# Performance work log

Hardware: AMD Instinct MI355X
Metric: run time of the kernel (lower is better)

## Reference

```python
import jax, jax.numpy as jnp
import numpy as np

N_DIM = 512
HIDDEN = 512


def setup_inputs() -> dict:
    key = jax.random.key(0)
    ks = jax.random.split(key, 9)
    s = 0.02
    x = jax.random.normal(ks[0], (4, 4096, N_DIM), dtype=jnp.float32)
    Wq = jax.random.normal(ks[1], (N_DIM, HIDDEN), dtype=jnp.float32) * s
    bq = jnp.zeros((HIDDEN,), dtype=jnp.float32)
    Wk = jax.random.normal(ks[2], (N_DIM, HIDDEN), dtype=jnp.float32) * s
    bk = jnp.zeros((HIDDEN,), dtype=jnp.float32)
    Wv = jax.random.normal(ks[3], (N_DIM, HIDDEN), dtype=jnp.float32) * s
    bv = jnp.zeros((HIDDEN,), dtype=jnp.float32)
    Wo = jax.random.normal(ks[4], (HIDDEN, N_DIM), dtype=jnp.float32) * s
    bo = jnp.zeros((N_DIM,), dtype=jnp.float32)
    return {"x": x, "Wq": Wq, "bq": bq, "Wk": Wk, "bk": bk,
            "Wv": Wv, "bv": bv, "Wo": Wo, "bo": bo}


def reference(x, Wq, bq, Wk, bk, Wv, bv, Wo, bo):
    # x: [B, S, n_dim]
    q = jnp.einsum('bsd,dh->bsh', x, Wq) + bq  # [B,S,H]
    k = jnp.einsum('bsd,dh->bsh', x, Wk) + bk
    v = jnp.einsum('bsd,dh->bsh', x, Wv) + bv
    # NOTE: original module uses UNSCALED scores (no 1/sqrt(d))
    scores = jnp.einsum('bqh,bkh->bqk', q, k)  # [B,S,S]
    attn = jax.nn.softmax(scores, axis=-1)
    y = jnp.einsum('bqk,bkh->bqh', attn, v)
    return jnp.einsum('bsh,hd->bsd', y, Wo) + bo
```

## Files before the change

kernel.cpp:

```cpp
#include <hip/hip_runtime.h>
#include <hip/hip_bf16.h>

typedef _Float16 h8 __attribute__((ext_vector_type(8)));
typedef __bf16   b8 __attribute__((ext_vector_type(8)));
typedef float    f4 __attribute__((ext_vector_type(4)));

#define B_    4
#define S_    4096
#define D_    512
#define ROWS_ (B_ * S_)
#define NQKV_ 1536
#define BR    64
#define BC2   64
#define NIT2  (S_ / BC2)
#define KP3   520
#define KT3   (BC2 * KP3)
#define PP3   72
#define YP    520
#define MSH   (30.0f * 1.4426950408889634f)
#define L2E   1.4426950408889634f

__device__ __forceinline__ void gl_lds16(const void* src, void* dst) {
    __builtin_amdgcn_global_load_lds(
        (const __attribute__((address_space(1))) unsigned int*)src,
        (__attribute__((address_space(3))) unsigned int*)dst, 16, 0, 0);
}

__global__ __launch_bounds__(256) void convert_all(
    const float* __restrict__ x,
    const float* __restrict__ Wq, const float* __restrict__ Wk, const float* __restrict__ Wv,
    const float* __restrict__ bq, const float* __restrict__ bk, const float* __restrict__ bv,
    const float* __restrict__ Wo,
    _Float16* __restrict__ xh, _Float16* __restrict__ wqkvT, _Float16* __restrict__ woT,
    float* __restrict__ bqkv)
{
    long i0 = (long)blockIdx.x * blockDim.x + threadIdx.x;
    long stride = (long)gridDim.x * blockDim.x;
    const long NX  = (long)ROWS_ * D_;
    const long NW  = (long)D_ * NQKV_;
    const long NWO = (long)D_ * D_;

    for (long i = i0; i < NX; i += stride) xh[i] = (_Float16)x[i];

    for (long i = i0; i < NW; i += stride) {
        long n = i >> 9, k = i & 511;
        long which = n >> 9, nn = n & 511;
        const float* W = (which == 0) ? Wq : (which == 1) ? Wk : Wv;
        wqkvT[i] = (_Float16)W[k * 512 + nn];
    }
    for (long i = i0; i < NWO; i += stride) {
        long n = i >> 9, k = i & 511;
        woT[i] = (_Float16)Wo[k * 512 + n];
    }
    for (long i = i0; i < NQKV_; i += stride) {
        long which = i >> 9, nn = i & 511;
        const float* bb = (which == 0) ? bq : (which == 1) ? bk : bv;
        bqkv[i] = bb[nn];
    }
}

template <bool OUT_F16>
__global__ __launch_bounds__(512) void gemm_bt(
    const _Float16* __restrict__ A, const _Float16* __restrict__ BT,
    const float* __restrict__ bias, void* __restrict__ Cout,
    int M, int N, int K, __bf16* __restrict__ vPout)
{
    __shared__ _Float16 As[2][128 * 32];
    __shared__ _Float16 Bs[2][256 * 32];

    int tid = threadIdx.x;
    int w = tid >> 6, lane = tid & 63, quad = lane >> 4, l16 = lane & 15;
    long row0 = (long)blockIdx.x * 128, col0 = (long)blockIdx.y * 256;
    int wr = (w >> 2) * 64, wc = (w & 3) * 64;

    f4 acc[4][4];
    for (int i = 0; i < 4; i++)
        for (int j = 0; j < 4; j++) acc[i][j] = (f4){0.f, 0.f, 0.f, 0.f};

    const int lrow = lane >> 2;
    const int lcol = (lane & 3) * 8;
    const int NT = K >> 5;

    gl_lds16(A  + (row0 + w * 16 + lrow) * K + lcol,        As[0] + w * 512);
    gl_lds16(BT + (col0 + w * 16 + lrow) * K + lcol,        Bs[0] + w * 512);
    gl_lds16(BT + (col0 + (w + 8) * 16 + lrow) * K + lcol,  Bs[0] + (w + 8) * 512);
    __syncthreads();

    for (int t = 0; t < NT; ++t) {
        const int cur = t & 1;
        if (t + 1 < NT) {
            const int k1 = (t + 1) * 32;
            gl_lds16(A  + (row0 + w * 16 + lrow) * K + k1 + lcol,        As[cur ^ 1] + w * 512);
            gl_lds16(BT + (col0 + w * 16 + lrow) * K + k1 + lcol,        Bs[cur ^ 1] + w * 512);
            gl_lds16(BT + (col0 + (w + 8) * 16 + lrow) * K + k1 + lcol,  Bs[cur ^ 1] + (w + 8) * 512);
        }
        h8 af[4], bf[4];
        for (int i = 0; i < 4; i++) af[i] = *(const h8*)(As[cur] + (wr + i * 16 + l16) * 32 + quad * 8);
        for (int j = 0; j < 4; j++) bf[j] = *(const h8*)(Bs[cur] + (wc + j * 16 + l16) * 32 + quad * 8);
        for (int i = 0; i < 4; i++)
            for (int j = 0; j < 4; j++)
                acc[i][j] = __builtin_amdgcn_mfma_f32_16x16x32_f16(af[i], bf[j], acc[i][j], 0, 0, 0);
        __builtin_amdgcn_sched_barrier(0);
        asm volatile("s_waitcnt vmcnt(0)");
        asm volatile("s_waitcnt lgkmcnt(0)");
        __builtin_amdgcn_s_barrier();
        __builtin_amdgcn_sched_barrier(0);
    }

    if (OUT_F16 && vPout != nullptr && col0 >= 1024) {
        for (int i = 0; i < 4; i++) {
            long row = row0 + wr + i * 16 + quad * 4;
            int bb   = (int)(row >> 12);
            int s    = (int)(row & 4095);
            int kt32 = s >> 5;
            int qq   = (s >> 3) & 3;
            int k3   = s & 7;
            for (int j = 0; j < 4; j++) {
                int dglob = (int)(col0 - 1024) + wc + j * 16;
                int dt = dglob >> 4;
                long off = (((long)bb * 128 + kt32) * 32 + dt) * 512
                         + (qq * 16 + l16) * 8 + k3;
                union { __bf16 h[4]; uint2 u2; } pk;
                for (int r = 0; r < 4; r++)
                    pk.h[r] = (__bf16)(acc[i][j][r] + bias[col0 + wc + j * 16 + l16]);
                *(uint2*)(vPout + off) = pk.u2;
            }
        }
    } else {
        for (int i = 0; i < 4; i++)
            for (int j = 0; j < 4; j++)
                for (int r = 0; r < 4; r++) {
                    long row = row0 + wr + i * 16 + quad * 4 + r;
                    long col = col0 + wc + j * 16 + l16;
                    float v = acc[i][j][r] + bias[col];
                    if (OUT_F16) ((_Float16*)Cout)[row * N + col] = (_Float16)v;
                    else         ((float*)Cout)[row * N + col]    = v;
                }
    }
}

__global__ __launch_bounds__(512, 2) void attn_kernel(const _Float16* __restrict__ qkv,
                                                      const __bf16* __restrict__ vP,
                                                      const _Float16* __restrict__ woT,
                                                      const float* __restrict__ bo,
                                                      float* __restrict__ out)
{
    __shared__ _Float16 Ks[2 * KT3];
    __shared__ __bf16   Ps[2 * BR * PP3];
    __shared__ float    lpart[2][BR];

    const int tid = threadIdx.x;
    const int w = tid >> 6, lane = tid & 63, quad = lane >> 4, l16 = lane & 15;

    const int bid = blockIdx.x;
    const int xcd = bid & 7;
    const int b = xcd >> 1;
    const long q0 = (long)((xcd & 1) * 32 + (bid >> 3)) * BR;
    const long rowBase = (long)b * S_;

    const _Float16* kbase = qkv + rowBase * NQKV_ + 512;

#pragma unroll
    for (int i = 0; i < 8; i++) {
        int r = w * 8 + i;
        gl_lds16(kbase + (long)r * NQKV_ + lane * 8, Ks + r * KP3);
    }

    if (w < 4) {
        const int rs0 = (w & 1) * 32;
        const int kg0 = (w >> 1) * 32;

        h8 Qf0[16], Qf1[16];
        {
            const _Float16* q0p = qkv + (rowBase + q0 + rs0 + l16) * NQKV_;
            const _Float16* q1p = q0p + 16 * NQKV_;
#pragma unroll
            for (int ks = 0; ks < 16; ks++) {
                Qf0[ks] = *(const h8*)(q0p + ks * 32 + quad * 8);
                Qf1[ks] = *(const h8*)(q1p + ks * 32 + quad * 8);
            }
        }
        float lo0[4] = {0.f, 0.f, 0.f, 0.f};
        float lo1[4] = {0.f, 0.f, 0.f, 0.f};

        __syncthreads();

        for (int kt = 0; kt < NIT2; kt++) {
            if (kt + 1 < NIT2) {
                const _Float16* kn = kbase + (long)(kt + 1) * BC2 * NQKV_;
                _Float16* kd = Ks + ((kt + 1) & 1) * KT3;
#pragma unroll
                for (int i = 0; i < 8; i++) {
                    int r = w * 8 + i;
                    gl_lds16(kn + (long)r * NQKV_ + lane * 8, kd + r * KP3);
                }
            }
            f4 S[2][2][2];
#pragma unroll
            for (int a = 0; a < 2; a++)
#pragma unroll
                for (int c = 0; c < 2; c++)
#pragma unroll
                    for (int d = 0; d < 2; d++) S[a][c][d] = (f4){0.f, 0.f, 0.f, 0.f};
            const _Float16* kr0 = Ks + (kt & 1) * KT3 + (kg0 + l16) * KP3 + quad * 8;
            const _Float16* kr1 = kr0 + 16 * KP3;
            __builtin_amdgcn_s_setprio(1);
#pragma unroll
            for (int ks = 0; ks < 8; ks++) {
                h8 a0 = *(const h8*)(kr0 + ks * 32);
                h8 a1 = *(const h8*)(kr0 + (ks + 8) * 32);
                h8 c0 = *(const h8*)(kr1 + ks * 32);
                h8 c1 = *(const h8*)(kr1 + (ks + 8) * 32);
                S[0][0][0] = __builtin_amdgcn_mfma_f32_16x16x32_f16(Qf0[ks],     a0, S[0][0][0], 0, 0, 0);
                S[1][0][0] = __builtin_amdgcn_mfma_f32_16x16x32_f16(Qf1[ks],     a0, S[1][0][0], 0, 0, 0);
                S[0][1][0] = __builtin_amdgcn_mfma_f32_16x16x32_f16(Qf0[ks],     c0, S[0][1][0], 0, 0, 0);
                S[1][1][0] = __builtin_amdgcn_mfma_f32_16x16x32_f16(Qf1[ks],     c0, S[1][1][0], 0, 0, 0);
                S[0][0][1] = __builtin_amdgcn_mfma_f32_16x16x32_f16(Qf0[ks + 8], a1, S[0][0][1], 0, 0, 0);
                S[1][0][1] = __builtin_amdgcn_mfma_f32_16x16x32_f16(Qf1[ks + 8], a1, S[1][0][1], 0, 0, 0);
                S[0][1][1] = __builtin_amdgcn_mfma_f32_16x16x32_f16(Qf0[ks + 8], c1, S[0][1][1], 0, 0, 0);
                S[1][1][1] = __builtin_amdgcn_mfma_f32_16x16x32_f16(Qf1[ks + 8], c1, S[1][1][1], 0, 0, 0);
            }
            __builtin_amdgcn_s_setprio(0);
            __bf16* ps = Ps + (kt & 1) * (BR * PP3);
#pragma unroll
            for (int r = 0; r < 4; r++) {
                float p00 = exp2f((S[0][0][0][r] + S[0][0][1][r]) * L2E - MSH);
                float p01 = exp2f((S[0][1][0][r] + S[0][1][1][r]) * L2E - MSH);
                float p10 = exp2f((S[1][0][0][r] + S[1][0][1][r]) * L2E - MSH);
                float p11 = exp2f((S[1][1][0][r] + S[1][1][1][r]) * L2E - MSH);
                __bf16 b00 = (__bf16)p00, b01 = (__bf16)p01;
                __bf16 b10 = (__bf16)p10, b11 = (__bf16)p11;
                int r0 = (rs0 + quad * 4 + r) * PP3;
                int r1 = (rs0 + 16 + quad * 4 + r) * PP3;
                ps[r0 + kg0 + l16]      = b00;
                ps[r0 + kg0 + 16 + l16] = b01;
                ps[r1 + kg0 + l16]      = b10;
                ps[r1 + kg0 + 16 + l16] = b11;
                lo0[r] += (float)b00 + (float)b01;
                lo1[r] += (float)b10 + (float)b11;
            }
            __builtin_amdgcn_sched_barrier(0);
            asm volatile("s_waitcnt vmcnt(0)");
            asm volatile("s_waitcnt lgkmcnt(0)");
            __builtin_amdgcn_s_barrier();
            __builtin_amdgcn_sched_barrier(0);
        }

#pragma unroll
        for (int r = 0; r < 4; r++)
#pragma unroll
            for (int m = 1; m < 16; m <<= 1) {
                lo0[r] += __shfl_xor(lo0[r], m, 16);
                lo1[r] += __shfl_xor(lo1[r], m, 16);
            }
        if (l16 == 0)
            for (int r = 0; r < 4; r++) {
                lpart[w >> 1][rs0 + quad * 4 + r]      = lo0[r];
                lpart[w >> 1][rs0 + 16 + quad * 4 + r] = lo1[r];
            }
        __syncthreads();
        __syncthreads();
    } else {
        const int cv = w - 4;
        const __bf16* vpbase = vP + ((long)b * 128 * 32 + cv * 8) * 512 + lane * 8;

        f4 O[4][8];
#pragma unroll
        for (int rt = 0; rt < 4; rt++)
#pragma unroll
            for (int ct = 0; ct < 8; ct++) O[rt][ct] = (f4){0.f, 0.f, 0.f, 0.f};
        b8 vreg[16];

        __syncthreads();

        for (int kt = 0; kt < NIT2; kt++) {
            if (kt + 1 < NIT2) {
                const _Float16* kn = kbase + (long)(kt + 1) * BC2 * NQKV_;
                _Float16* kd = Ks + ((kt + 1) & 1) * KT3;
#pragma unroll
                for (int i = 0; i < 8; i++) {
                    int r = w * 8 + i;
                    gl_lds16(kn + (long)r * NQKV_ + lane * 8, kd + r * KP3);
                }
            }
            __builtin_amdgcn_sched_barrier(0);
            if (kt > 0) {
                if (kt < NIT2 - 1) asm volatile("s_waitcnt vmcnt(8)");
                else               asm volatile("s_waitcnt vmcnt(0)");
                const __bf16* ps = Ps + ((kt - 1) & 1) * (BR * PP3);
                __builtin_amdgcn_s_setprio(1);
#pragma unroll
                for (int rt = 0; rt < 4; rt++) {
                    b8 pa0 = *(const b8*)(ps + (rt * 16 + l16) * PP3 + quad * 8);
                    b8 pa1 = *(const b8*)(ps + (rt * 16 + l16) * PP3 + 32 + quad * 8);
#pragma unroll
                    for (int ct = 0; ct < 8; ct++) {
                        O[rt][ct] = __builtin_amdgcn_mfma_f32_16x16x32_bf16(pa0, vreg[ct],     O[rt][ct], 0, 0, 0);
                        O[rt][ct] = __builtin_amdgcn_mfma_f32_16x16x32_bf16(pa1, vreg[8 + ct], O[rt][ct], 0, 0, 0);
                    }
                }
                __builtin_amdgcn_s_setprio(0);
            }
            {
                const __bf16* vs0 = vpbase + (long)(2 * kt) * (32 * 512);
#pragma unroll
                for (int ct = 0; ct < 8; ct++) {
                    vreg[ct]     = *(const b8*)(vs0 + ct * 512);
                    vreg[8 + ct] = *(const b8*)(vs0 + 32 * 512 + ct * 512);
                }
            }
            __builtin_amdgcn_sched_barrier(0);
            asm volatile("s_waitcnt vmcnt(16)");
            asm volatile("s_waitcnt lgkmcnt(0)");
            __builtin_amdgcn_s_barrier();
            __builtin_amdgcn_sched_barrier(0);
        }
        asm volatile("s_waitcnt vmcnt(0)");
        {
            const __bf16* ps = Ps + ((NIT2 - 1) & 1) * (BR * PP3);
#pragma unroll
            for (int rt = 0; rt < 4; rt++) {
                b8 pa0 = *(const b8*)(ps + (rt * 16 + l16) * PP3 + quad * 8);
                b8 pa1 = *(const b8*)(ps + (rt * 16 + l16) * PP3 + 32 + quad * 8);
#pragma unroll
                for (int ct = 0; ct < 8; ct++) {
                    O[rt][ct] = __builtin_amdgcn_mfma_f32_16x16x32_bf16(pa0, vreg[ct],     O[rt][ct], 0, 0, 0);
                    O[rt][ct] = __builtin_amdgcn_mfma_f32_16x16x32_bf16(pa1, vreg[8 + ct], O[rt][ct], 0, 0, 0);
                }
            }
        }
        __syncthreads();

        {
            _Float16* y_lds = Ks;
#pragma unroll
            for (int rt = 0; rt < 4; rt++) {
                f4 l0 = *(const f4*)(&lpart[0][rt * 16 + quad * 4]);
                f4 l1 = *(const f4*)(&lpart[1][rt * 16 + quad * 4]);
                float li[4];
                for (int r = 0; r < 4; r++) li[r] = 1.f / (l0[r] + l1[r]);
                for (int ct = 0; ct < 8; ct++)
                    for (int r = 0; r < 4; r++)
                        y_lds[(rt * 16 + quad * 4 + r) * YP + cv * 128 + ct * 16 + l16] =
                            (_Float16)(O[rt][ct][r] * li[r]);
            }
        }
        __syncthreads();
    }

    {
        const _Float16* y_lds = Ks;
        f4 acc[4][4];
#pragma unroll
        for (int i = 0; i < 4; i++)
#pragma unroll
            for (int j = 0; j < 4; j++) acc[i][j] = (f4){0.f, 0.f, 0.f, 0.f};
        const _Float16* wb = woT + (long)(w * 64 + l16) * 512 + quad * 8;
#pragma unroll
        for (int ks = 0; ks < 16; ks++) {
            h8 af[4], bf[4];
#pragma unroll
            for (int i = 0; i < 4; i++)
                af[i] = *(const h8*)(y_lds + (i * 16 + l16) * YP + ks * 32 + quad * 8);
#pragma unroll
            for (int j = 0; j < 4; j++)
                bf[j] = *(const h8*)(wb + (long)j * 16 * 512 + ks * 32);
#pragma unroll
            for (int i = 0; i < 4; i++)
#pragma unroll
                for (int j = 0; j < 4; j++)
                    acc[i][j] = __builtin_amdgcn_mfma_f32_16x16x32_f16(af[i], bf[j], acc[i][j], 0, 0, 0);
        }
#pragma unroll
        for (int i = 0; i < 4; i++)
#pragma unroll
            for (int j = 0; j < 4; j++)
                for (int r = 0; r < 4; r++) {
                    long row = rowBase + q0 + i * 16 + quad * 4 + r;
                    int col = w * 64 + j * 16 + l16;
                    out[row * 512 + col] = acc[i][j][r] + bo[col];
                }
    }
}

extern "C" void kernel_launch(void* const* d_in, const int* in_sizes, int n_in,
                              void* d_out, int out_size, void* d_ws, size_t ws_size,
                              hipStream_t stream)
{
    const float* x  = (const float*)d_in[0];
    const float* Wq = (const float*)d_in[1];
    const float* bq = (const float*)d_in[2];
    const float* Wk = (const float*)d_in[3];
    const float* bk = (const float*)d_in[4];
    const float* Wv = (const float*)d_in[5];
    const float* bv = (const float*)d_in[6];
    const float* Wo = (const float*)d_in[7];
    const float* bo = (const float*)d_in[8];
    float* out = (float*)d_out;

    char* ws = (char*)d_ws;
    _Float16* xh    = (_Float16*)(ws);
    _Float16* qkv   = (_Float16*)(ws + 16777216);
    __bf16*   vP    = (__bf16*)(ws + 67108864);
    _Float16* wqkvT = (_Float16*)(ws + 100663296);
    _Float16* woT   = (_Float16*)(ws + 102236160);
    float*    bqkv  = (float*)(ws + 102760448);

    convert_all<<<2048, 256, 0, stream>>>(x, Wq, Wk, Wv, bq, bk, bv, Wo,
                                          xh, wqkvT, woT, bqkv);

    dim3 g1(128, 6);
    gemm_bt<true><<<g1, 512, 0, stream>>>(xh, wqkvT, bqkv, qkv, ROWS_, NQKV_, D_, vP);

    attn_kernel<<<256, 512, 0, stream>>>(qkv, vP, woT, bo, out);
}
```

Measured before the change: 295.7 us.

## Fuse convert, QKV GEMM and attention into one cooperative persistent kernel

Merges the three separate launches (conversion, QKV projection GEMM, attention plus output projection) into a single cooperative kernel of 256 blocks, separated by grid-wide syncs. This removes launch gaps and kernel-boundary drains between stages. In exchange, the GEMM stage now runs 768 tiles over 256 persistent blocks with a large static LDS allocation, and the conversion stage uses fewer threads. Grid syncs add their own overhead.

```diff
diff --git a/kernel.cpp b/kernel.cpp
--- a/kernel.cpp
+++ b/kernel.cpp
@@ -1,5 +1,8 @@
 #include <hip/hip_runtime.h>
 #include <hip/hip_bf16.h>
+#include <hip/hip_cooperative_groups.h>
+
+namespace cg = cooperative_groups;
 
 typedef _Float16 h8 __attribute__((ext_vector_type(8)));
 typedef __bf16   b8 __attribute__((ext_vector_type(8)));
@@ -26,269 +29,307 @@
         (__attribute__((address_space(3))) unsigned int*)dst, 16, 0, 0);
 }
 
-__global__ __launch_bounds__(256) void convert_all(
+__global__ __launch_bounds__(512, 2) void fused_all(
     const float* __restrict__ x,
-    const float* __restrict__ Wq, const float* __restrict__ Wk, const float* __restrict__ Wv,
-    const float* __restrict__ bq, const float* __restrict__ bk, const float* __restrict__ bv,
-    const float* __restrict__ Wo,
-    _Float16* __restrict__ xh, _Float16* __restrict__ wqkvT, _Float16* __restrict__ woT,
-    float* __restrict__ bqkv)
+    const float* __restrict__ Wq, const float* __restrict__ bq,
+    const float* __restrict__ Wk, const float* __restrict__ bk,
+    const float* __restrict__ Wv, const float* __restrict__ bv,
+    const float* __restrict__ Wo, const float* __restrict__ bo,
+    _Float16* __restrict__ xh, _Float16* __restrict__ wqkvT,
+    _Float16* __restrict__ woT, float* __restrict__ bqkv,
+    _Float16* __restrict__ qkv, __bf16* __restrict__ vP,
+    float* __restrict__ out)
 {
-    long i0 = (long)blockIdx.x * blockDim.x + threadIdx.x;
-    long stride = (long)gridDim.x * blockDim.x;
-    const long NX  = (long)ROWS_ * D_;
-    const long NW  = (long)D_ * NQKV_;
-    const long NWO = (long)D_ * D_;
-
-    for (long i = i0; i < NX; i += stride) xh[i] = (_Float16)x[i];
-
-    for (long i = i0; i < NW; i += stride) {
-        long n = i >> 9, k = i & 511;
-        long which = n >> 9, nn = n & 511;
-        const float* W = (which == 0) ? Wq : (which == 1) ? Wk : Wv;
-        wqkvT[i] = (_Float16)W[k * 512 + nn];
+    __shared__ __align__(16) char smem[152064];
+
+    cg::grid_group gg = cg::this_grid();
+    const int tid = threadIdx.x;
+    const int bid = blockIdx.x;
+    const int w = tid >> 6, lane = tid & 63, quad = lane >> 4, l16 = lane & 15;
+
+    {
+        long i0 = (long)bid * 512 + tid;
+        const long stride = 256 * 512;
+        const long NX  = (long)ROWS_ * D_;
+        const long NW  = (long)D_ * NQKV_;
+        const long NWO = (long)D_ * D_;
+
+        for (long i = i0; i < NX; i += stride) xh[i] = (_Float16)x[i];
+
+        for (long i = i0; i < NW; i += stride) {
+            long n = i >> 9, k = i & 511;
+            long which = n >> 9, nn = n & 511;
+            const float* W = (which == 0) ? Wq : (which == 1) ? Wk : Wv;
+            wqkvT[i] = (_Float16)W[k * 512 + nn];
+        }
+        for (long i = i0; i < NWO; i += stride) {
+            long n = i >> 9, k = i & 511;
+            woT[i] = (_Float16)Wo[k * 512 + n];
+        }
+        for (long i = i0; i < NQKV_; i += stride) {
+            long which = i >> 9, nn = i & 511;
+            const float* bb = (which == 0) ? bq : (which == 1) ? bk : bv;
+            bqkv[i] = bb[nn];
+        }
     }
-    for (long i = i0; i < NWO; i += stride) {
-        long n = i >> 9, k = i & 511;
-        woT[i] = (_Float16)Wo[k * 512 + n];
+    __threadfence();
+    gg.sync();
+
+    {
+        _Float16* As = (_Float16*)smem;
+        _Float16* Bs = (_Float16*)(smem + 16384);
+        const int lrow = lane >> 2;
+        const int lcol = (lane & 3) * 8;
+        const int wr = (w >> 2) * 64, wc = (w & 3) * 64;
+
+        for (int tile = bid; tile < 768; tile += 256) {
+            const long row0 = (long)(tile & 127) * 128;
+            const long col0 = (long)(tile >> 7) * 256;
+
+            f4 acc[4][4];
+#pragma unroll
+            for (int i = 0; i < 4; i++)
+#pragma unroll
+                for (int j = 0; j < 4; j++) acc[i][j] = (f4){0.f, 0.f, 0.f, 0.f};
+
+            gl_lds16(xh    + (row0 + w * 16 + lrow) * 512 + lcol,       As + w * 512);
+            gl_lds16(wqkvT + (col0 + w * 16 + lrow) * 512 + lcol,       Bs + w * 512);
+            gl_lds16(wqkvT + (col0 + (w + 8) * 16 + lrow) * 512 + lcol, Bs + (w + 8) * 512);
+            __syncthreads();
+
+            for (int t = 0; t < 16; ++t) {
+                const int cur = t & 1;
+                if (t + 1 < 16) {
+                    const int k1 = (t + 1) * 32;
+                    gl_lds16(xh    + (row0 + w * 16 + lrow) * 512 + k1 + lcol,       As + (cur ^ 1) * 4096 + w * 512);
+                    gl_lds16(wqkvT + (col0 + w * 16 + lrow) * 512 + k1 + lcol,       Bs + (cur ^ 1) * 8192 + w * 512);
+                    gl_lds16(wqkvT + (col0 + (w + 8) * 16 + lrow) * 512 + k1 + lcol, Bs + (cur ^ 1) * 8192 + (w + 8) * 512);
+                }
+                h8 af[4], bf[4];
+#pragma unroll
+                for (int i = 0; i < 4; i++) af[i] = *(const h8*)(As + cur * 4096 + (wr + i * 16 + l16) * 32 + quad * 8);
+#pragma unroll
+                for (int j = 0; j < 4; j++) bf[j] = *(const h8*)(Bs + cur * 8192 + (wc + j * 16 + l16) * 32 + quad * 8);
+#pragma unroll
+                for (int i = 0; i < 4; i++)
+#pragma unroll
+                    for (int j = 0; j < 4; j++)
+                        acc[i][j] = __builtin_amdgcn_mfma_f32_16x16x32_f16(af[i], bf[j], acc[i][j], 0, 0, 0);
+                __builtin_amdgcn_sched_barrier(0);
+                asm volatile("s_waitcnt vmcnt(0)");
+                asm volatile("s_waitcnt lgkmcnt(0)");
+                __builtin_amdgcn_s_barrier();
+                __builtin_amdgcn_sched_barrier(0);
+            }
+
+            if (col0 >= 1024) {
+#pragma unroll
+                for (int i = 0; i < 4; i++) {
+                    long row = row0 + wr + i * 16 + quad * 4;
+                    int bb   = (int)(row >> 12);
+                    int s    = (int)(row & 4095);
+                    int kt32 = s >> 5;
+                    int qq   = (s >> 3) & 3;
+                    int k3   = s & 7;
+#pragma unroll
+                    for (int j = 0; j < 4; j++) {
+                        int dglob = (int)(col0 - 1024) + wc + j * 16;
+                        int dt = dglob >> 4;
+                        long off = (((long)bb * 128 + kt32) * 32 + dt) * 512
+                                 + (qq * 16 + l16) * 8 + k3;
+                        union { __bf16 h[4]; uint2 u2; } pk;
+                        for (int r = 0; r < 4; r++)
+                            pk.h[r] = (__bf16)(acc[i][j][r] + bqkv[col0 + wc + j * 16 + l16]);
+                        *(uint2*)(vP + off) = pk.u2;
+                    }
+                }
+            } else {
+#pragma unroll
+                for (int i = 0; i < 4; i++)
+#pragma unroll
+                    for (int j = 0; j < 4; j++)
+                        for (int r = 0; r < 4; r++) {
+                            long row = row0 + wr + i * 16 + quad * 4 + r;
+                            long col = col0 + wc + j * 16 + l16;
+                            qkv[row * NQKV_ + col] = (_Float16)(acc[i][j][r] + bqkv[col]);
+                        }
+            }
+            __syncthreads();
+        }
     }
-    for (long i = i0; i < NQKV_; i += stride) {
-        long which = i >> 9, nn = i & 511;
-        const float* bb = (which == 0) ? bq : (which == 1) ? bk : bv;
-        bqkv[i] = bb[nn];
-    }
-}
-
-template <bool OUT_F16>
-__global__ __launch_bounds__(512) void gemm_bt(
-    const _Float16* __restrict__ A, const _Float16* __restrict__ BT,
-    const float* __restrict__ bias, void* __restrict__ Cout,
-    int M, int N, int K, __bf16* __restrict__ vPout)
-{
-    __shared__ _Float16 As[2][128 * 32];
-    __shared__ _Float16 Bs[2][256 * 32];
-
-    int tid = threadIdx.x;
-    int w = tid >> 6, lane = tid & 63, quad = lane >> 4, l16 = lane & 15;
-    long row0 = (long)blockIdx.x * 128, col0 = (long)blockIdx.y * 256;
-    int wr = (w >> 2) * 64, wc = (w & 3) * 64;
-
-    f4 acc[4][4];
-    for (int i = 0; i < 4; i++)
-        for (int j = 0; j < 4; j++) acc[i][j] = (f4){0.f, 0.f, 0.f, 0.f};
-
-    const int lrow = lane >> 2;
-    const int lcol = (lane & 3) * 8;
-    const int NT = K >> 5;
-
-    gl_lds16(A  + (row0 + w * 16 + lrow) * K + lcol,        As[0] + w * 512);
-    gl_lds16(BT + (col0 + w * 16 + lrow) * K + lcol,        Bs[0] + w * 512);
-    gl_lds16(BT + (col0 + (w + 8) * 16 + lrow) * K + lcol,  Bs[0] + (w + 8) * 512);
-    __syncthreads();
-
-    for (int t = 0; t < NT; ++t) {
-        const int cur = t & 1;
-        if (t + 1 < NT) {
-            const int k1 = (t + 1) * 32;
-            gl_lds16(A  + (row0 + w * 16 + lrow) * K + k1 + lcol,        As[cur ^ 1] + w * 512);
-            gl_lds16(BT + (col0 + w * 16 + lrow) * K + k1 + lcol,        Bs[cur ^ 1] + w * 512);
-            gl_lds16(BT + (col0 + (w + 8) * 16 + lrow) * K + k1 + lcol,  Bs[cur ^ 1] + (w + 8) * 512);
-        }
-        h8 af[4], bf[4];
-        for (int i = 0; i < 4; i++) af[i] = *(const h8*)(As[cur] + (wr + i * 16 + l16) * 32 + quad * 8);
-        for (int j = 0; j < 4; j++) bf[j] = *(const h8*)(Bs[cur] + (wc + j * 16 + l16) * 32 + quad * 8);
-        for (int i = 0; i < 4; i++)
-            for (int j = 0; j < 4; j++)
-                acc[i][j] = __builtin_amdgcn_mfma_f32_16x16x32_f16(af[i], bf[j], acc[i][j], 0, 0, 0);
-        __builtin_amdgcn_sched_barrier(0);
-        asm volatile("s_waitcnt vmcnt(0)");
-        asm volatile("s_waitcnt lgkmcnt(0)");
-        __builtin_amdgcn_s_barrier();
-        __builtin_amdgcn_sched_barrier(0);
-    }
-
-    if (OUT_F16 && vPout != nullptr && col0 >= 1024) {
-        for (int i = 0; i < 4; i++) {
-            long row = row0 + wr + i * 16 + quad * 4;
-            int bb   = (int)(row >> 12);
-            int s    = (int)(row & 4095);
-            int kt32 = s >> 5;
-            int qq   = (s >> 3) & 3;
-            int k3   = s & 7;
-            for (int j = 0; j < 4; j++) {
-                int dglob = (int)(col0 - 1024) + wc + j * 16;
-                int dt = dglob >> 4;
-                long off = (((long)bb * 128 + kt32) * 32 + dt) * 512
-                         + (qq * 16 + l16) * 8 + k3;
-                union { __bf16 h[4]; uint2 u2; } pk;
-                for (int r = 0; r < 4; r++)
-                    pk.h[r] = (__bf16)(acc[i][j][r] + bias[col0 + wc + j * 16 + l16]);
-                *(uint2*)(vPout + off) = pk.u2;
-            }
-        }
-    } else {
-        for (int i = 0; i < 4; i++)
-            for (int j = 0; j < 4; j++)
+    __threadfence();
+    gg.sync();
+
+    {
+        _Float16* Ks = (_Float16*)smem;
+        __bf16*   Ps = (__bf16*)(smem + 133120);
+        float*    lp = (float*)(smem + 151552);
+
+        const int xcd = bid & 7;
+        const int b = xcd >> 1;
+        const long q0 = (long)((xcd & 1) * 32 + (bid >> 3)) * BR;
+        const long rowBase = (long)b * S_;
+
+        const _Float16* kbase = qkv + rowBase * NQKV_ + 512;
+
+#pragma unroll
+        for (int i = 0; i < 8; i++) {
+            int r = w * 8 + i;
+            gl_lds16(kbase + (long)r * NQKV_ + lane * 8, Ks + r * KP3);
+        }
+
+        if (w < 4) {
+            const int rs0 = (w & 1) * 32;
+            const int kg0 = (w >> 1) * 32;
+
+            h8 Qf0[16], Qf1[16];
+            {
+                const _Float16* q0p = qkv + (rowBase + q0 + rs0 + l16) * NQKV_;
+                const _Float16* q1p = q0p + 16 * NQKV_;
+#pragma unroll
+                for (int ks = 0; ks < 16; ks++) {
+                    Qf0[ks] = *(const h8*)(q0p + ks * 32 + quad * 8);
+                    Qf1[ks] = *(const h8*)(q1p + ks * 32 + quad * 8);
+                }
+            }
+            float lo0[4] = {0.f, 0.f, 0.f, 0.f};
+            float lo1[4] = {0.f, 0.f, 0.f, 0.f};
+
+            __syncthreads();
+
+            for (int kt = 0; kt < NIT2; kt++) {
+                if (kt + 1 < NIT2) {
+                    const _Float16* kn = kbase + (long)(kt + 1) * BC2 * NQKV_;
+                    _Float16* kd = Ks + ((kt + 1) & 1) * KT3;
+#pragma unroll
+                    for (int i = 0; i < 8; i++) {
+                        int r = w * 8 + i;
+                        gl_lds16(kn + (long)r * NQKV_ + lane * 8, kd + r * KP3);
+                    }
+                }
+                f4 S[2][2][2];
+#pragma unroll
+                for (int a = 0; a < 2; a++)
+#pragma unroll
+                    for (int c = 0; c < 2; c++)
+#pragma unroll
+                        for (int d = 0; d < 2; d++) S[a][c][d] = (f4){0.f, 0.f, 0.f, 0.f};
+                const _Float16* kr0 = Ks + (kt & 1) * KT3 + (kg0 + l16) * KP3 + quad * 8;
+                const _Float16* kr1 = kr0 + 16 * KP3;
+                __builtin_amdgcn_s_setprio(1);
+#pragma unroll
+                for (int ks = 0; ks < 8; ks++) {
+                    h8 a0 = *(const h8*)(kr0 + ks * 32);
+                    h8 a1 = *(const h8*)(kr0 + (ks + 8) * 32);
+                    h8 c0 = *(const h8*)(kr1 + ks * 32);
+                    h8 c1 = *(const h8*)(kr1 + (ks + 8) * 32);
+                    S[0][0][0] = __builtin_amdgcn_mfma_f32_16x16x32_f16(Qf0[ks],     a0, S[0][0][0], 0, 0, 0);
+                    S[1][0][0] = __builtin_amdgcn_mfma_f32_16x16x32_f16(Qf1[ks],     a0, S[1][0][0], 0, 0, 0);
+                    S[0][1][0] = __builtin_amdgcn_mfma_f32_16x16x32_f16(Qf0[ks],     c0, S[0][1][0], 0, 0, 0);
+                    S[1][1][0] = __builtin_amdgcn_mfma_f32_16x16x32_f16(Qf1[ks],     c0, S[1][1][0], 0, 0, 0);
+                    S[0][0][1] = __builtin_amdgcn_mfma_f32_16x16x32_f16(Qf0[ks + 8], a1, S[0][0][1], 0, 0, 0);
+                    S[1][0][1] = __builtin_amdgcn_mfma_f32_16x16x32_f16(Qf1[ks + 8], a1, S[1][0][1], 0, 0, 0);
+                    S[0][1][1] = __builtin_amdgcn_mfma_f32_16x16x32_f16(Qf0[ks + 8], c1, S[0][1][1], 0, 0, 0);
+                    S[1][1][1] = __builtin_amdgcn_mfma_f32_16x16x32_f16(Qf1[ks + 8], c1, S[1][1][1], 0, 0, 0);
+                }
+                __builtin_amdgcn_s_setprio(0);
+                __bf16* ps = Ps + (kt & 1) * (BR * PP3);
+#pragma unroll
                 for (int r = 0; r < 4; r++) {
-                    long row = row0 + wr + i * 16 + quad * 4 + r;
-                    long col = col0 + wc + j * 16 + l16;
-                    float v = acc[i][j][r] + bias[col];
-                    if (OUT_F16) ((_Float16*)Cout)[row * N + col] = (_Float16)v;
-                    else         ((float*)Cout)[row * N + col]    = v;
-                }
-    }
-}
-
-__global__ __launch_bounds__(512, 2) void attn_kernel(const _Float16* __restrict__ qkv,
-                                                      const __bf16* __restrict__ vP,
-                                                      const _Float16* __restrict__ woT,
-                                                      const float* __restrict__ bo,
-                                                      float* __restrict__ out)
-{
-    __shared__ _Float16 Ks[2 * KT3];
-    __shared__ __bf16   Ps[2 * BR * PP3];
-    __shared__ float    lpart[2][BR];
-
-    const int tid = threadIdx.x;
-    const int w = tid >> 6, lane = tid & 63, quad = lane >> 4, l16 = lane & 15;
-
-    const int bid = blockIdx.x;
-    const int xcd = bid & 7;
-    const int b = xcd >> 1;
-    const long q0 = (long)((xcd & 1) * 32 + (bid >> 3)) * BR;
-    const long rowBase = (long)b * S_;
-
-    const _Float16* kbase = qkv + rowBase * NQKV_ + 512;
-
-#pragma unroll
-    for (int i = 0; i < 8; i++) {
-        int r = w * 8 + i;
-        gl_lds16(kbase + (long)r * NQKV_ + lane * 8, Ks + r * KP3);
-    }
-
-    if (w < 4) {
-        const int rs0 = (w & 1) * 32;
-        const int kg0 = (w >> 1) * 32;
-
-        h8 Qf0[16], Qf1[16];
-        {
-            const _Float16* q0p = qkv + (rowBase + q0 + rs0 + l16) * NQKV_;
-            const _Float16* q1p = q0p + 16 * NQKV_;
-#pragma unroll
-            for (int ks = 0; ks < 16; ks++) {
-                Qf0[ks] = *(const h8*)(q0p + ks * 32 + quad * 8);
-                Qf1[ks] = *(const h8*)(q1p + ks * 32 + quad * 8);
-            }
-        }
-        float lo0[4] = {0.f, 0.f, 0.f, 0.f};
-        float lo1[4] = {0.f, 0.f, 0.f, 0.f};
-
-        __syncthreads();
-
-        for (int kt = 0; kt < NIT2; kt++) {
-            if (kt + 1 < NIT2) {
-                const _Float16* kn = kbase + (long)(kt + 1) * BC2 * NQKV_;
-                _Float16* kd = Ks + ((kt + 1) & 1) * KT3;
-#pragma unroll
-                for (int i = 0; i < 8; i++) {
-                    int r = w * 8 + i;
-                    gl_lds16(kn + (long)r * NQKV_ + lane * 8, kd + r * KP3);
-                }
-            }
-            f4 S[2][2][2];
-#pragma unroll
-            for (int a = 0; a < 2; a++)
-#pragma unroll
-                for (int c = 0; c < 2; c++)
-#pragma unroll
-                    for (int d = 0; d < 2; d++) S[a][c][d] = (f4){0.f, 0.f, 0.f, 0.f};
-            const _Float16* kr0 = Ks + (kt & 1) * KT3 + (kg0 + l16) * KP3 + quad * 8;
-            const _Float16* kr1 = kr0 + 16 * KP3;
-            __builtin_amdgcn_s_setprio(1);
-#pragma unroll
-            for (int ks = 0; ks < 8; ks++) {
-                h8 a0 = *(const h8*)(kr0 + ks * 32);
-                h8 a1 = *(const h8*)(kr0 + (ks + 8) * 32);
-                h8 c0 = *(const h8*)(kr1 + ks * 32);
-                h8 c1 = *(const h8*)(kr1 + (ks + 8) * 32);
-                S[0][0][0] = __builtin_amdgcn_mfma_f32_16x16x32_f16(Qf0[ks],     a0, S[0][0][0], 0, 0, 0);
-                S[1][0][0] = __builtin_amdgcn_mfma_f32_16x16x32_f16(Qf1[ks],     a0, S[1][0][0], 0, 0, 0);
-                S[0][1][0] = __builtin_amdgcn_mfma_f32_16x16x32_f16(Qf0[ks],     c0, S[0][1][0], 0, 0, 0);
-                S[1][1][0] = __builtin_amdgcn_mfma_f32_16x16x32_f16(Qf1[ks],     c0, S[1][1][0], 0, 0, 0);
-                S[0][0][1] = __builtin_amdgcn_mfma_f32_16x16x32_f16(Qf0[ks + 8], a1, S[0][0][1], 0, 0, 0);
-                S[1][0][1] = __builtin_amdgcn_mfma_f32_16x16x32_f16(Qf1[ks + 8], a1, S[1][0][1], 0, 0, 0);
-                S[0][1][1] = __builtin_amdgcn_mfma_f32_16x16x32_f16(Qf0[ks + 8], c1, S[0][1][1], 0, 0, 0);
-                S[1][1][1] = __builtin_amdgcn_mfma_f32_16x16x32_f16(Qf1[ks + 8], c1, S[1][1][1], 0, 0, 0);
-            }
-            __builtin_amdgcn_s_setprio(0);
-            __bf16* ps = Ps + (kt & 1) * (BR * PP3);
-#pragma unroll
-            for (int r = 0; r < 4; r++) {
-                float p00 = exp2f((S[0][0][0][r] + S[0][0][1][r]) * L2E - MSH);
-                float p01 = exp2f((S[0][1][0][r] + S[0][1][1][r]) * L2E - MSH);
-                float p10 = exp2f((S[1][0][0][r] + S[1][0][1][r]) * L2E - MSH);
-                float p11 = exp2f((S[1][1][0][r] + S[1][1][1][r]) * L2E - MSH);
-                __bf16 b00 = (__bf16)p00, b01 = (__bf16)p01;
-                __bf16 b10 = (__bf16)p10, b11 = (__bf16)p11;
-                int r0 = (rs0 + quad * 4 + r) * PP3;
-                int r1 = (rs0 + 16 + quad * 4 + r) * PP3;
-                ps[r0 + kg0 + l16]      = b00;
-                ps[r0 + kg0 + 16 + l16] = b01;
-                ps[r1 + kg0 + l16]      = b10;
-                ps[r1 + kg0 + 16 + l16] = b11;
-                lo0[r] += (float)b00 + (float)b01;
-                lo1[r] += (float)b10 + (float)b11;
-            }
-            __builtin_amdgcn_sched_barrier(0);
+                    float p00 = exp2f((S[0][0][0][r] + S[0][0][1][r]) * L2E - MSH);
+                    float p01 = exp2f((S[0][1][0][r] + S[0][1][1][r]) * L2E - MSH);
+                    float p10 = exp2f((S[1][0][0][r] + S[1][0][1][r]) * L2E - MSH);
+                    float p11 = exp2f((S[1][1][0][r] + S[1][1][1][r]) * L2E - MSH);
+                    __bf16 b00 = (__bf16)p00, b01 = (__bf16)p01;
+                    __bf16 b10 = (__bf16)p10, b11 = (__bf16)p11;
+                    int r0 = (rs0 + quad * 4 + r) * PP3;
+                    int r1 = (rs0 + 16 + quad * 4 + r) * PP3;
+                    ps[r0 + kg0 + l16]      = b00;
+                    ps[r0 + kg0 + 16 + l16] = b01;
+                    ps[r1 + kg0 + l16]      = b10;
+                    ps[r1 + kg0 + 16 + l16] = b11;
+                    lo0[r] += (float)b00 + (float)b01;
+                    lo1[r] += (float)b10 + (float)b11;
+                }
+                __builtin_amdgcn_sched_barrier(0);
+                asm volatile("s_waitcnt vmcnt(0)");
+                asm volatile("s_waitcnt lgkmcnt(0)");
+                __builtin_amdgcn_s_barrier();
+                __builtin_amdgcn_sched_barrier(0);
+            }
+
+#pragma unroll
+            for (int r = 0; r < 4; r++)
+#pragma unroll
+                for (int m = 1; m < 16; m <<= 1) {
+                    lo0[r] += __shfl_xor(lo0[r], m, 16);
+                    lo1[r] += __shfl_xor(lo1[r], m, 16);
+                }
+            if (l16 == 0)
+                for (int r = 0; r < 4; r++) {
+                    lp[(w >> 1) * 64 + rs0 + quad * 4 + r]      = lo0[r];
+                    lp[(w >> 1) * 64 + rs0 + 16 + quad * 4 + r] = lo1[r];
+                }
+            __syncthreads();
+            __syncthreads();
+        } else {
+            const int cv = w - 4;
+            const __bf16* vpbase = vP + ((long)b * 128 * 32 + cv * 8) * 512 + lane * 8;
+
+            f4 O[4][8];
+#pragma unroll
+            for (int rt = 0; rt < 4; rt++)
+#pragma unroll
+                for (int ct = 0; ct < 8; ct++) O[rt][ct] = (f4){0.f, 0.f, 0.f, 0.f};
+            b8 vreg[16];
+
+            __syncthreads();
+
+            for (int kt = 0; kt < NIT2; kt++) {
+                if (kt + 1 < NIT2) {
+                    const _Float16* kn = kbase + (long)(kt + 1) * BC2 * NQKV_;
+                    _Float16* kd = Ks + ((kt + 1) & 1) * KT3;
+#pragma unroll
+                    for (int i = 0; i < 8; i++) {
+                        int r = w * 8 + i;
+                        gl_lds16(kn + (long)r * NQKV_ + lane * 8, kd + r * KP3);
+                    }
+                }
+                __builtin_amdgcn_sched_barrier(0);
+                if (kt > 0) {
+                    if (kt < NIT2 - 1) asm volatile("s_waitcnt vmcnt(8)");
+                    else               asm volatile("s_waitcnt vmcnt(0)");
+                    const __bf16* ps = Ps + ((kt - 1) & 1) * (BR * PP3);
+                    __builtin_amdgcn_s_setprio(1);
+#pragma unroll
+                    for (int rt = 0; rt < 4; rt++) {
+                        b8 pa0 = *(const b8*)(ps + (rt * 16 + l16) * PP3 + quad * 8);
+                        b8 pa1 = *(const b8*)(ps + (rt * 16 + l16) * PP3 + 32 + quad * 8);
+#pragma unroll
+                        for (int ct = 0; ct < 8; ct++) {
+                            O[rt][ct] = __builtin_amdgcn_mfma_f32_16x16x32_bf16(pa0, vreg[ct],     O[rt][ct], 0, 0, 0);
+                            O[rt][ct] = __builtin_amdgcn_mfma_f32_16x16x32_bf16(pa1, vreg[8 + ct], O[rt][ct], 0, 0, 0);
+                        }
+                    }
+                    __builtin_amdgcn_s_setprio(0);
+                }
+                {
+                    const __bf16* vs0 = vpbase + (long)(2 * kt) * (32 * 512);
+#pragma unroll
+                    for (int ct = 0; ct < 8; ct++) {
+                        vreg[ct]     = *(const b8*)(vs0 + ct * 512);
+                        vreg[8 + ct] = *(const b8*)(vs0 + 32 * 512 + ct * 512);
+                    }
+                }
+                __builtin_amdgcn_sched_barrier(0);
+                asm volatile("s_waitcnt vmcnt(16)");
+                asm volatile("s_waitcnt lgkmcnt(0)");
+                __builtin_amdgcn_s_barrier();
+                __builtin_amdgcn_sched_barrier(0);
+            }
             asm volatile("s_waitcnt vmcnt(0)");
-            asm volatile("s_waitcnt lgkmcnt(0)");
-            __builtin_amdgcn_s_barrier();
-            __builtin_amdgcn_sched_barrier(0);
-        }
-
-#pragma unroll
-        for (int r = 0; r < 4; r++)
-#pragma unroll
-            for (int m = 1; m < 16; m <<= 1) {
-                lo0[r] += __shfl_xor(lo0[r], m, 16);
-                lo1[r] += __shfl_xor(lo1[r], m, 16);
-            }
-        if (l16 == 0)
-            for (int r = 0; r < 4; r++) {
-                lpart[w >> 1][rs0 + quad * 4 + r]      = lo0[r];
-                lpart[w >> 1][rs0 + 16 + quad * 4 + r] = lo1[r];
-            }
-        __syncthreads();
-        __syncthreads();
-    } else {
-        const int cv = w - 4;
-        const __bf16* vpbase = vP + ((long)b * 128 * 32 + cv * 8) * 512 + lane * 8;
-
-        f4 O[4][8];
-#pragma unroll
-        for (int rt = 0; rt < 4; rt++)
-#pragma unroll
-            for (int ct = 0; ct < 8; ct++) O[rt][ct] = (f4){0.f, 0.f, 0.f, 0.f};
-        b8 vreg[16];
-
-        __syncthreads();
-
-        for (int kt = 0; kt < NIT2; kt++) {
-            if (kt + 1 < NIT2) {
-                const _Float16* kn = kbase + (long)(kt + 1) * BC2 * NQKV_;
-                _Float16* kd = Ks + ((kt + 1) & 1) * KT3;
-#pragma unroll
-                for (int i = 0; i < 8; i++) {
-                    int r = w * 8 + i;
-                    gl_lds16(kn + (long)r * NQKV_ + lane * 8, kd + r * KP3);
-                }
-            }
-            __builtin_amdgcn_sched_barrier(0);
-            if (kt > 0) {
-                if (kt < NIT2 - 1) asm volatile("s_waitcnt vmcnt(8)");
-                else               asm volatile("s_waitcnt vmcnt(0)");
-                const __bf16* ps = Ps + ((kt - 1) & 1) * (BR * PP3);
-                __builtin_amdgcn_s_setprio(1);
+            {
+                const __bf16* ps = Ps + ((NIT2 - 1) & 1) * (BR * PP3);
 #pragma unroll
                 for (int rt = 0; rt < 4; rt++) {
                     b8 pa0 = *(const b8*)(ps + (rt * 16 + l16) * PP3 + quad * 8);
@@ -299,87 +340,59 @@
                         O[rt][ct] = __builtin_amdgcn_mfma_f32_16x16x32_bf16(pa1, vreg[8 + ct], O[rt][ct], 0, 0, 0);
                     }
                 }
-                __builtin_amdgcn_s_setprio(0);
-            }
+            }
+            __syncthreads();
+
             {
-                const __bf16* vs0 = vpbase + (long)(2 * kt) * (32 * 512);
-#pragma unroll
-                for (int ct = 0; ct < 8; ct++) {
-                    vreg[ct]     = *(const b8*)(vs0 + ct * 512);
-                    vreg[8 + ct] = *(const b8*)(vs0 + 32 * 512 + ct * 512);
-                }
-            }
-            __builtin_amdgcn_sched_barrier(0);
-            asm volatile("s_waitcnt vmcnt(16)");
-            asm volatile("s_waitcnt lgkmcnt(0)");
-            __builtin_amdgcn_s_barrier();
-            __builtin_amdgcn_sched_barrier(0);
-        }
-        asm volatile("s_waitcnt vmcnt(0)");
+                _Float16* y_lds = Ks;
+#pragma unroll
+                for (int rt = 0; rt < 4; rt++) {
+                    f4 l0 = *(const f4*)(lp + rt * 16 + quad * 4);
+                    f4 l1 = *(const f4*)(lp + 64 + rt * 16 + quad * 4);
+                    float li[4];
+                    for (int r = 0; r < 4; r++) li[r] = 1.f / (l0[r] + l1[r]);
+                    for (int ct = 0; ct < 8; ct++)
+                        for (int r = 0; r < 4; r++)
+                            y_lds[(rt * 16 + quad * 4 + r) * YP + cv * 128 + ct * 16 + l16] =
+                                (_Float16)(O[rt][ct][r] * li[r]);
+                }
+            }
+            __syncthreads();
+        }
+
         {
-            const __bf16* ps = Ps + ((NIT2 - 1) & 1) * (BR * PP3);
-#pragma unroll
-            for (int rt = 0; rt < 4; rt++) {
-                b8 pa0 = *(const b8*)(ps + (rt * 16 + l16) * PP3 + quad * 8);
-                b8 pa1 = *(const b8*)(ps + (rt * 16 + l16) * PP3 + 32 + quad * 8);
-#pragma unroll
-                for (int ct = 0; ct < 8; ct++) {
-                    O[rt][ct] = __builtin_amdgcn_mfma_f32_16x16x32_bf16(pa0, vreg[ct],     O[rt][ct], 0, 0, 0);
-                    O[rt][ct] = __builtin_amdgcn_mfma_f32_16x16x32_bf16(pa1, vreg[8 + ct], O[rt][ct], 0, 0, 0);
-                }
-            }
-        }
-        __syncthreads();
-
-        {
-            _Float16* y_lds = Ks;
-#pragma unroll
-            for (int rt = 0; rt < 4; rt++) {
-                f4 l0 = *(const f4*)(&lpart[0][rt * 16 + quad * 4]);
-                f4 l1 = *(const f4*)(&lpart[1][rt * 16 + quad * 4]);
-                float li[4];
-                for (int r = 0; r < 4; r++) li[r] = 1.f / (l0[r] + l1[r]);
-                for (int ct = 0; ct < 8; ct++)
-                    for (int r = 0; r < 4; r++)
-                        y_lds[(rt * 16 + quad * 4 + r) * YP + cv * 128 + ct * 16 + l16] =
-                            (_Float16)(O[rt][ct][r] * li[r]);
-            }
-        }
-        __syncthreads();
-    }
-
-    {
-        const _Float16* y_lds = Ks;
-        f4 acc[4][4];
-#pragma unroll
-        for (int i = 0; i < 4; i++)
-#pragma unroll
-            for (int j = 0; j < 4; j++) acc[i][j] = (f4){0.f, 0.f, 0.f, 0.f};
-        const _Float16* wb = woT + (long)(w * 64 + l16) * 512 + quad * 8;
-#pragma unroll
-        for (int ks = 0; ks < 16; ks++) {
-            h8 af[4], bf[4];
+            const _Float16* y_lds = Ks;
+            f4 acc[4][4];
 #pragma unroll
             for (int i = 0; i < 4; i++)
-                af[i] = *(const h8*)(y_lds + (i * 16 + l16) * YP + ks * 32 + quad * 8);
-#pragma unroll
-            for (int j = 0; j < 4; j++)
-                bf[j] = *(const h8*)(wb + (long)j * 16 * 512 + ks * 32);
+#pragma unroll
+                for (int j = 0; j < 4; j++) acc[i][j] = (f4){0.f, 0.f, 0.f, 0.f};
+            const _Float16* wb = woT + (long)(w * 64 + l16) * 512 + quad * 8;
+#pragma unroll
+            for (int ks = 0; ks < 16; ks++) {
+                h8 af[4], bf[4];
+#pragma unroll
+                for (int i = 0; i < 4; i++)
+                    af[i] = *(const h8*)(y_lds + (i * 16 + l16) * YP + ks * 32 + quad * 8);
+#pragma unroll
+                for (int j = 0; j < 4; j++)
+                    bf[j] = *(const h8*)(wb + (long)j * 16 * 512 + ks * 32);
+#pragma unroll
+                for (int i = 0; i < 4; i++)
+#pragma unroll
+                    for (int j = 0; j < 4; j++)
+                        acc[i][j] = __builtin_amdgcn_mfma_f32_16x16x32_f16(af[i], bf[j], acc[i][j], 0, 0, 0);
+            }
 #pragma unroll
             for (int i = 0; i < 4; i++)
 #pragma unroll
                 for (int j = 0; j < 4; j++)
-                    acc[i][j] = __builtin_amdgcn_mfma_f32_16x16x32_f16(af[i], bf[j], acc[i][j], 0, 0, 0);
-        }
-#pragma unroll
-        for (int i = 0; i < 4; i++)
-#pragma unroll
-            for (int j = 0; j < 4; j++)
-                for (int r = 0; r < 4; r++) {
-                    long row = rowBase + q0 + i * 16 + quad * 4 + r;
-                    int col = w * 64 + j * 16 + l16;
-                    out[row * 512 + col] = acc[i][j][r] + bo[col];
-                }
+                    for (int r = 0; r < 4; r++) {
+                        long row = rowBase + q0 + i * 16 + quad * 4 + r;
+                        int col = w * 64 + j * 16 + l16;
+                        out[row * 512 + col] = acc[i][j][r] + bo[col];
+                    }
+        }
     }
 }
 
@@ -406,11 +419,12 @@
     _Float16* woT   = (_Float16*)(ws + 102236160);
     float*    bqkv  = (float*)(ws + 102760448);
 
-    convert_all<<<2048, 256, 0, stream>>>(x, Wq, Wk, Wv, bq, bk, bv, Wo,
-                                          xh, wqkvT, woT, bqkv);
-
-    dim3 g1(128, 6);
-    gemm_bt<true><<<g1, 512, 0, stream>>>(xh, wqkvT, bqkv, qkv, ROWS_, NQKV_, D_, vP);
-
-    attn_kernel<<<256, 512, 0, stream>>>(qkv, vP, woT, bo, out);
+    void* args[] = {
+        (void*)&x, (void*)&Wq, (void*)&bq, (void*)&Wk, (void*)&bk,
+        (void*)&Wv, (void*)&bv, (void*)&Wo, (void*)&bo,
+        (void*)&xh, (void*)&wqkvT, (void*)&woT, (void*)&bqkv,
+        (void*)&qkv, (void*)&vP, (void*)&out
+    };
+    hipLaunchCooperativeKernel((const void*)fused_all, dim3(256), dim3(512),
+                               args, 0, stream);
 }
```

Measured after the change: 479.3 us. 62.1% more time.
